# Kernel tuning notes

Measured on AMD Instinct MI355X. Metric: run time of the kernel, lower is better.

## Reference

```python
import jax, jax.numpy as jnp
import numpy as np

B, H, W, C = 4, 256, 256, 256
WS = 8          # window size (both dims)
HEADS = 1
SEQ = WS * WS   # 64 tokens per window
NW = B * (H // WS) * (W // WS)  # 4096 windows
INNER = C * HEADS


def setup_inputs() -> dict:
    key = jax.random.key(0)
    k1, k2, k3, k4 = jax.random.split(key, 4)
    x = jax.random.normal(k1, (B, H, W, C), dtype=jnp.float32)
    attn = jax.random.uniform(k2, (NW, HEADS, SEQ, SEQ), dtype=jnp.float32)
    # to_v: Linear(dim, inner_dim, bias=False); stored as [in, out] for x @ Wv
    Wv = jax.random.normal(k3, (C, INNER), dtype=jnp.float32) * (C ** -0.5)
    # to_out: Linear(inner_dim, dim)
    Wo = jax.random.normal(k4, (INNER, C), dtype=jnp.float32) * (INNER ** -0.5)
    bo = jnp.zeros((C,), dtype=jnp.float32)
    return {"x": x, "attn": attn, "Wv": Wv, "Wo": Wo, "bo": bo}


def reference(x, attn, Wv, Wo, bo):
    b, h, w, c = x.shape
    nh, nw = h // WS, w // WS
    # window partition: b (h b0) (w b1) c -> (b h w) (b0 b1) c
    xw = x.reshape(b, nh, WS, nw, WS, c).transpose(0, 1, 3, 2, 4, 5)
    xw = xw.reshape(b * nh * nw, SEQ, c)
    # value projection, split heads: n s (h d) -> n h s d
    v = (xw @ Wv).reshape(-1, SEQ, HEADS, c).transpose(0, 2, 1, 3)
    # precomputed-attention weighted sum
    out = jnp.einsum('nhij,nhjd->nhid', attn, v)
    # merge heads: n h s d -> n s (h d)
    out = out.transpose(0, 2, 1, 3).reshape(-1, SEQ, HEADS * c)
    out = out @ Wo + bo
    # window un-partition: (b h w) (b0 b1) c -> b (h b0) (w b1) c
    out = out.reshape(b, nh, nw, WS, WS, c).transpose(0, 1, 3, 2, 4, 5)
    return out.reshape(b, h, w, c)
```

## Files before the change

kernel.cpp:

```cpp
#include <hip/hip_runtime.h>
#include <hip/hip_bf16.h>


typedef __bf16 bf16x8 __attribute__((ext_vector_type(8)));
typedef __bf16 bf16x4 __attribute__((ext_vector_type(4)));
typedef float  f32x16 __attribute__((ext_vector_type(16)));
typedef float  f32x4  __attribute__((ext_vector_type(4)));
typedef unsigned int uint;
typedef uint   uint4v __attribute__((ext_vector_type(4)));

#define MFMA32(a, b, c) __builtin_amdgcn_mfma_f32_32x32x16_bf16(a, b, c, 0, 0, 0)

__global__ void wfuse_kernel(const float* __restrict__ Wv,
                             const float* __restrict__ Wo,
                             __bf16* __restrict__ WT) {
  const int n = blockIdx.x;
  const int k = threadIdx.x;
  const float* wvrow = Wv + k * 256;
  float acc = 0.f;
#pragma unroll 4
  for (int j = 0; j < 256; j += 4) {
    f32x4 wv = *(const f32x4*)(wvrow + j);
    acc += wv.x * Wo[(j + 0) * 256 + n];
    acc += wv.y * Wo[(j + 1) * 256 + n];
    acc += wv.z * Wo[(j + 2) * 256 + n];
    acc += wv.w * Wo[(j + 3) * 256 + n];
  }
  WT[n * 256 + k] = (__bf16)acc;
}

static __device__ __forceinline__ uint pkbf(float lo, float hi) {
  return (uint)__builtin_bit_cast(unsigned short, (__bf16)lo) |
         ((uint)__builtin_bit_cast(unsigned short, (__bf16)hi) << 16);
}

static __device__ __forceinline__ void build_bfrags(const f32x16 acc, int lh,
                                                    bf16x8* bf) {
  uint wd0 = pkbf(acc[0],  acc[1]);
  uint wd1 = pkbf(acc[2],  acc[3]);
  uint wd2 = pkbf(acc[4],  acc[5]);
  uint wd3 = pkbf(acc[6],  acc[7]);
  uint wd4 = pkbf(acc[8],  acc[9]);
  uint wd5 = pkbf(acc[10], acc[11]);
  uint wd6 = pkbf(acc[12], acc[13]);
  uint wd7 = pkbf(acc[14], acc[15]);
  {
    uint o0 = (uint)__shfl_xor((int)wd2, 32);
    uint o1 = (uint)__shfl_xor((int)wd3, 32);
    uint o2 = (uint)__shfl_xor((int)wd0, 32);
    uint o3 = (uint)__shfl_xor((int)wd1, 32);
    uint4v uv = { lh ? o0 : wd0, lh ? o1 : wd1,
                  lh ? wd2 : o2, lh ? wd3 : o3 };
    bf[0] = __builtin_bit_cast(bf16x8, uv);
  }
  {
    uint o0 = (uint)__shfl_xor((int)wd6, 32);
    uint o1 = (uint)__shfl_xor((int)wd7, 32);
    uint o2 = (uint)__shfl_xor((int)wd4, 32);
    uint o3 = (uint)__shfl_xor((int)wd5, 32);
    uint4v uv = { lh ? o0 : wd4, lh ? o1 : wd5,
                  lh ? wd6 : o2, lh ? wd7 : o3 };
    bf[1] = __builtin_bit_cast(bf16x8, uv);
  }
}

static __device__ __forceinline__ long wbase(int w) {
  int wi = w & 31;
  int hi = (w >> 5) & 31;
  int b  = w >> 10;
  return (((long)(b * 256 + hi * 8)) * 256 + wi * 8) * 256;
}

__global__ __launch_bounds__(512, 2)
void na_msa_kernel(const float* __restrict__ x,
                   const float* __restrict__ attn,
                   const __bf16* __restrict__ WT,
                   const float* __restrict__ bo,
                   float* __restrict__ out) {
  __shared__ char lds[81920];

  const int t    = threadIdx.x;
  const int lane = t & 63;
  const int wvi  = t >> 6;
  const int ln31 = lane & 31;
  const int lh   = lane >> 5;

  const __bf16* wtp = WT + (wvi * 32 + ln31) * 256 + 8 * lh;
  const float bv = bo[wvi * 32 + ln31];

  const int tq   = t >> 6;
  const int xch0 = (t & 63) * 4;
  const int arow0 = t >> 4;
  const int ak0   = (t & 15) * 4;

  const int w0 = blockIdx.x * 16;

#define XBYT(J)  ((((J) * 8 + tq) * 512) + ((xch0 * 2) ^ ((((J) * 8 + tq) & 31) << 4)))
#define CVT4(V)  bf16x4{ (__bf16)(V).x, (__bf16)(V).y, (__bf16)(V).z, (__bf16)(V).w }

#define AWR(BAT, R0, R1) do {                                              \
    *(bf16x4*)((BAT) + arow0 * 128 + ((ak0 * 2) ^ ((arow0 & 7) << 4))) =   \
        bf16x4{ (__bf16)(R0).x, (__bf16)(R0).y, (__bf16)(R0).z, (__bf16)(R0).w }; \
    int row1_ = 32 + arow0;                                                \
    *(bf16x4*)((BAT) + row1_ * 128 + ((ak0 * 2) ^ ((row1_ & 7) << 4))) =   \
        bf16x4{ (__bf16)(R1).x, (__bf16)(R1).y, (__bf16)(R1).z, (__bf16)(R1).w }; \
    } while (0)

  bf16x8 wb[16];
#pragma unroll
  for (int ks = 0; ks < 16; ++ks) wb[ks] = *(const bf16x8*)(wtp + ks * 16);

  {
    const float* xp = x + wbase(w0);
    const float* ap = attn + (long)w0 * 4096;
    f32x4 v0 = *(const f32x4*)(xp + 0 * 65536 + t * 4);
    f32x4 v1 = *(const f32x4*)(xp + 1 * 65536 + t * 4);
    f32x4 v2 = *(const f32x4*)(xp + 2 * 65536 + t * 4);
    f32x4 v3 = *(const f32x4*)(xp + 3 * 65536 + t * 4);
    f32x4 v4 = *(const f32x4*)(xp + 4 * 65536 + t * 4);
    f32x4 v5 = *(const f32x4*)(xp + 5 * 65536 + t * 4);
    f32x4 v6 = *(const f32x4*)(xp + 6 * 65536 + t * 4);
    f32x4 v7 = *(const f32x4*)(xp + 7 * 65536 + t * 4);
    f32x4 a0 = *(const f32x4*)(ap + t * 4);
    f32x4 a1 = *(const f32x4*)(ap + (512 + t) * 4);
    *(bf16x4*)(lds + XBYT(0)) = CVT4(v0);
    *(bf16x4*)(lds + XBYT(1)) = CVT4(v1);
    *(bf16x4*)(lds + XBYT(2)) = CVT4(v2);
    *(bf16x4*)(lds + XBYT(3)) = CVT4(v3);
    *(bf16x4*)(lds + XBYT(4)) = CVT4(v4);
    *(bf16x4*)(lds + XBYT(5)) = CVT4(v5);
    *(bf16x4*)(lds + XBYT(6)) = CVT4(v6);
    *(bf16x4*)(lds + XBYT(7)) = CVT4(v7);
    AWR(lds + 32768, a0, a1);
  }
  asm volatile("s_waitcnt lgkmcnt(0)" ::: "memory");
  __builtin_amdgcn_s_barrier();
  __builtin_amdgcn_sched_barrier(0);

#pragma unroll 1
  for (int i = 0; i < 16; ++i) {
    const int w = w0 + i;
    const char* xs = lds + (i & 1) * 40960;
    const char* as = xs + 32768;

    f32x4 px0, px1, px2, px3, px4, px5, px6, px7, pa0, pa1;
    if (i < 15) {
      const float* xp = x + wbase(w + 1);
      const float* ap = attn + (long)(w + 1) * 4096;
      px0 = *(const f32x4*)(xp + 0 * 65536 + t * 4);
      px1 = *(const f32x4*)(xp + 1 * 65536 + t * 4);
      px2 = *(const f32x4*)(xp + 2 * 65536 + t * 4);
      px3 = *(const f32x4*)(xp + 3 * 65536 + t * 4);
      px4 = *(const f32x4*)(xp + 4 * 65536 + t * 4);
      px5 = *(const f32x4*)(xp + 5 * 65536 + t * 4);
      px6 = *(const f32x4*)(xp + 6 * 65536 + t * 4);
      px7 = *(const f32x4*)(xp + 7 * 65536 + t * 4);
      pa0 = *(const f32x4*)(ap + t * 4);
      pa1 = *(const f32x4*)(ap + (512 + t) * 4);
    }
    __builtin_amdgcn_sched_barrier(0);

    f32x16 acc0 = {}, acc1 = {};
#pragma unroll
    for (int ks = 0; ks < 16; ++ks) {
      int kk = ks * 16 + 8 * lh;
      int byt0 = ln31 * 512 + ((kk * 2) ^ (ln31 << 4));
      bf16x8 a0 = *(const bf16x8*)(xs + byt0);
      bf16x8 a1 = *(const bf16x8*)(xs + byt0 + 16384);
      acc0 = MFMA32(a0, wb[ks], acc0);
      acc1 = MFMA32(a1, wb[ks], acc1);
    }

    bf16x8 bfr[4];
    build_bfrags(acc0, lh, &bfr[0]);
    build_bfrags(acc1, lh, &bfr[2]);

    float* op = out + wbase(w);
    const int ch = wvi * 32 + ln31;

    {
      f32x16 o0 = {};
#pragma unroll
      for (int ks = 0; ks < 4; ++ks) {
        int kk = ks * 16 + 8 * lh;
        int ab0 = ln31 * 128 + ((kk * 2) ^ ((ln31 & 7) << 4));
        bf16x8 a0 = *(const bf16x8*)(as + ab0);
        o0 = MFMA32(a0, bfr[ks], o0);
      }
#pragma unroll
      for (int r = 0; r < 16; ++r) {
        int tok = (r & 3) + 8 * (r >> 2) + 4 * lh;
        op[(tok >> 3) * 65536 + (tok & 7) * 256 + ch] = o0[r] + bv;
      }
    }
    {
      f32x16 o1 = {};
#pragma unroll
      for (int ks = 0; ks < 4; ++ks) {
        int kk = ks * 16 + 8 * lh;
        int ab0 = ln31 * 128 + ((kk * 2) ^ ((ln31 & 7) << 4));
        bf16x8 a1 = *(const bf16x8*)(as + ab0 + 4096);
        o1 = MFMA32(a1, bfr[ks], o1);
      }
#pragma unroll
      for (int r = 0; r < 16; ++r) {
        int tok = 32 + (r & 3) + 8 * (r >> 2) + 4 * lh;
        op[(tok >> 3) * 65536 + (tok & 7) * 256 + ch] = o1[r] + bv;
      }
    }

    if (i < 15) {
      char* bxw = lds + ((i + 1) & 1) * 40960;
      *(bf16x4*)(bxw + XBYT(0)) = CVT4(px0);
      *(bf16x4*)(bxw + XBYT(1)) = CVT4(px1);
      *(bf16x4*)(bxw + XBYT(2)) = CVT4(px2);
      *(bf16x4*)(bxw + XBYT(3)) = CVT4(px3);
      *(bf16x4*)(bxw + XBYT(4)) = CVT4(px4);
      *(bf16x4*)(bxw + XBYT(5)) = CVT4(px5);
      *(bf16x4*)(bxw + XBYT(6)) = CVT4(px6);
      *(bf16x4*)(bxw + XBYT(7)) = CVT4(px7);
      AWR(bxw + 32768, pa0, pa1);
    }

    asm volatile("s_waitcnt lgkmcnt(0)" ::: "memory");
    __builtin_amdgcn_s_barrier();
    __builtin_amdgcn_sched_barrier(0);
  }
#undef XBYT
#undef CVT4
#undef AWR
}

extern "C" void kernel_launch(void* const* d_in, const int* in_sizes, int n_in,
                              void* d_out, int out_size, void* d_ws, size_t ws_size,
                              hipStream_t stream) {
  const float* x    = (const float*)d_in[0];
  const float* attn = (const float*)d_in[1];
  const float* Wv   = (const float*)d_in[2];
  const float* Wo   = (const float*)d_in[3];
  const float* bo   = (const float*)d_in[4];
  float* out = (float*)d_out;
  __bf16* WT = (__bf16*)d_ws;

  wfuse_kernel<<<256, 256, 0, stream>>>(Wv, Wo, WT);
  na_msa_kernel<<<256, 512, 0, stream>>>(x, attn, WT, bo, out);
}
```

Measured before the change: 153.2 us.

## Split fused window kernel into projection and attention kernels via workspace

Replaces the single persistent, software-pipelined kernel (256 blocks, 16 windows each) with two kernels of one window per block. The first computes x·(Wv·Wo) in bf16 and writes the MFMA B-fragments to a 128 MB workspace. The second reads attn and those fragments and produces the output. This trades extra global traffic (writing and rereading the bf16 intermediate) for far more blocks and simpler per-block work, and it falls back to the fused kernel when the workspace is too small.

```diff
diff --git a/kernel.cpp b/kernel.cpp
--- a/kernel.cpp
+++ b/kernel.cpp
@@ -71,6 +71,142 @@
   return (((long)(b * 256 + hi * 8)) * 256 + wi * 8) * 256;
 }
 
+__global__ __launch_bounds__(512)
+void zprod_kernel(const float* __restrict__ x,
+                  const __bf16* __restrict__ WT,
+                  __bf16* __restrict__ zf) {
+  __shared__ char lds[32768];
+
+  const int t    = threadIdx.x;
+  const int lane = t & 63;
+  const int wvi  = t >> 6;
+  const int ln31 = lane & 31;
+  const int lh   = lane >> 5;
+
+  const int w = blockIdx.x;
+  const float* xp = x + wbase(w);
+
+  const int tq   = t >> 6;
+  const int xch0 = (t & 63) * 4;
+#define XBYT(J)  ((((J) * 8 + tq) * 512) + ((xch0 * 2) ^ ((((J) * 8 + tq) & 31) << 4)))
+#define CVT4(V)  bf16x4{ (__bf16)(V).x, (__bf16)(V).y, (__bf16)(V).z, (__bf16)(V).w }
+
+  f32x4 v0 = *(const f32x4*)(xp + 0 * 65536 + t * 4);
+  f32x4 v1 = *(const f32x4*)(xp + 1 * 65536 + t * 4);
+  f32x4 v2 = *(const f32x4*)(xp + 2 * 65536 + t * 4);
+  f32x4 v3 = *(const f32x4*)(xp + 3 * 65536 + t * 4);
+  f32x4 v4 = *(const f32x4*)(xp + 4 * 65536 + t * 4);
+  f32x4 v5 = *(const f32x4*)(xp + 5 * 65536 + t * 4);
+  f32x4 v6 = *(const f32x4*)(xp + 6 * 65536 + t * 4);
+  f32x4 v7 = *(const f32x4*)(xp + 7 * 65536 + t * 4);
+  *(bf16x4*)(lds + XBYT(0)) = CVT4(v0);
+  *(bf16x4*)(lds + XBYT(1)) = CVT4(v1);
+  *(bf16x4*)(lds + XBYT(2)) = CVT4(v2);
+  *(bf16x4*)(lds + XBYT(3)) = CVT4(v3);
+  *(bf16x4*)(lds + XBYT(4)) = CVT4(v4);
+  *(bf16x4*)(lds + XBYT(5)) = CVT4(v5);
+  *(bf16x4*)(lds + XBYT(6)) = CVT4(v6);
+  *(bf16x4*)(lds + XBYT(7)) = CVT4(v7);
+  __syncthreads();
+
+  const __bf16* wtp = WT + (wvi * 32 + ln31) * 256 + 8 * lh;
+  f32x16 acc0 = {}, acc1 = {};
+#pragma unroll
+  for (int ks = 0; ks < 16; ++ks) {
+    int kk = ks * 16 + 8 * lh;
+    int byt0 = ln31 * 512 + ((kk * 2) ^ (ln31 << 4));
+    bf16x8 a0 = *(const bf16x8*)(lds + byt0);
+    bf16x8 a1 = *(const bf16x8*)(lds + byt0 + 16384);
+    bf16x8 b0 = *(const bf16x8*)(wtp + ks * 16);
+    acc0 = MFMA32(a0, b0, acc0);
+    acc1 = MFMA32(a1, b0, acc1);
+  }
+
+  bf16x8 bfr[4];
+  build_bfrags(acc0, lh, &bfr[0]);
+  build_bfrags(acc1, lh, &bfr[2]);
+  __bf16* zp = zf + (((long)(w * 8 + wvi) * 4) << 9) + lane * 8;
+#pragma unroll
+  for (int ks = 0; ks < 4; ++ks) {
+    *(bf16x8*)(zp + (ks << 9)) = bfr[ks];
+  }
+#undef XBYT
+#undef CVT4
+}
+
+__global__ __launch_bounds__(512)
+void att_kernel(const float* __restrict__ attn,
+                const __bf16* __restrict__ zf,
+                const float* __restrict__ bo,
+                float* __restrict__ out) {
+  __shared__ char lds_at[8192];
+
+  const int t    = threadIdx.x;
+  const int lane = t & 63;
+  const int wvi  = t >> 6;
+  const int ln31 = lane & 31;
+  const int lh   = lane >> 5;
+
+  const int w = blockIdx.x;
+  const float* ap = attn + (long)w * 4096;
+
+  const int arow0 = t >> 4;
+  const int ak0   = (t & 15) * 4;
+
+  f32x4 a0 = *(const f32x4*)(ap + t * 4);
+  f32x4 a1 = *(const f32x4*)(ap + (512 + t) * 4);
+  const __bf16* zp = zf + (((long)(w * 8 + wvi) * 4) << 9) + lane * 8;
+  bf16x8 bfr[4];
+#pragma unroll
+  for (int ks = 0; ks < 4; ++ks) {
+    bfr[ks] = *(const bf16x8*)(zp + (ks << 9));
+  }
+
+  *(bf16x4*)(lds_at + arow0 * 128 + ((ak0 * 2) ^ ((arow0 & 7) << 4))) =
+      bf16x4{ (__bf16)a0.x, (__bf16)a0.y, (__bf16)a0.z, (__bf16)a0.w };
+  {
+    int row1 = 32 + arow0;
+    *(bf16x4*)(lds_at + row1 * 128 + ((ak0 * 2) ^ ((row1 & 7) << 4))) =
+        bf16x4{ (__bf16)a1.x, (__bf16)a1.y, (__bf16)a1.z, (__bf16)a1.w };
+  }
+  __syncthreads();
+
+  float* op = out + wbase(w);
+  const int ch = wvi * 32 + ln31;
+  const float bv = bo[ch];
+
+  {
+    f32x16 o0 = {};
+#pragma unroll
+    for (int ks = 0; ks < 4; ++ks) {
+      int kk = ks * 16 + 8 * lh;
+      int ab0 = ln31 * 128 + ((kk * 2) ^ ((ln31 & 7) << 4));
+      bf16x8 aa = *(const bf16x8*)(lds_at + ab0);
+      o0 = MFMA32(aa, bfr[ks], o0);
+    }
+#pragma unroll
+    for (int r = 0; r < 16; ++r) {
+      int tok = (r & 3) + 8 * (r >> 2) + 4 * lh;
+      op[(tok >> 3) * 65536 + (tok & 7) * 256 + ch] = o0[r] + bv;
+    }
+  }
+  {
+    f32x16 o1 = {};
+#pragma unroll
+    for (int ks = 0; ks < 4; ++ks) {
+      int kk = ks * 16 + 8 * lh;
+      int ab0 = ln31 * 128 + ((kk * 2) ^ ((ln31 & 7) << 4));
+      bf16x8 aa = *(const bf16x8*)(lds_at + ab0 + 4096);
+      o1 = MFMA32(aa, bfr[ks], o1);
+    }
+#pragma unroll
+    for (int r = 0; r < 16; ++r) {
+      int tok = 32 + (r & 3) + 8 * (r >> 2) + 4 * lh;
+      op[(tok >> 3) * 65536 + (tok & 7) * 256 + ch] = o1[r] + bv;
+    }
+  }
+}
+
 __global__ __launch_bounds__(512, 2)
 void na_msa_kernel(const float* __restrict__ x,
                    const float* __restrict__ attn,
@@ -97,7 +233,6 @@
 
 #define XBYT(J)  ((((J) * 8 + tq) * 512) + ((xch0 * 2) ^ ((((J) * 8 + tq) & 31) << 4)))
 #define CVT4(V)  bf16x4{ (__bf16)(V).x, (__bf16)(V).y, (__bf16)(V).z, (__bf16)(V).w }
-
 #define AWR(BAT, R0, R1) do {                                              \
     *(bf16x4*)((BAT) + arow0 * 128 + ((ak0 * 2) ^ ((arow0 & 7) << 4))) =   \
         bf16x4{ (__bf16)(R0).x, (__bf16)(R0).y, (__bf16)(R0).z, (__bf16)(R0).w }; \
@@ -177,7 +312,6 @@
 
     float* op = out + wbase(w);
     const int ch = wvi * 32 + ln31;
-
     {
       f32x16 o0 = {};
 #pragma unroll
@@ -241,7 +375,15 @@
   const float* bo   = (const float*)d_in[4];
   float* out = (float*)d_out;
   __bf16* WT = (__bf16*)d_ws;
+  __bf16* zf = (__bf16*)((char*)d_ws + 131072);
 
   wfuse_kernel<<<256, 256, 0, stream>>>(Wv, Wo, WT);
-  na_msa_kernel<<<256, 512, 0, stream>>>(x, attn, WT, bo, out);
-}
+
+  const size_t need = 131072 + (size_t)134217728;
+  if (ws_size >= need) {
+    zprod_kernel<<<4096, 512, 0, stream>>>(x, WT, zf);
+    att_kernel<<<4096, 512, 0, stream>>>(attn, zf, bo, out);
+  } else {
+    na_msa_kernel<<<256, 512, 0, stream>>>(x, attn, WT, bo, out);
+  }
+}
```

New measurement: 235.8 us. +53.9%, slower.
